# Performance work log

Hardware: AMD Instinct MI355X
Metric: run time of the kernel (lower is better)

Reference implementation:

```python
import jax, jax.numpy as jnp
import numpy as np

B, S, H = 1, 4096, 2048
HQ, HKV, D = 8, 4, 256
WIN = 1024          # sliding window
SOFTCAP = 50.0      # attn logit softcapping
EPS = 1e-6          # rms_norm_eps
ROPE_THETA = 10000.0


def setup_inputs() -> dict:
    key = jax.random.key(0)
    ks = jax.random.split(key, 6)
    hidden_states = jax.random.normal(ks[0], (B, S, H), dtype=jnp.float32)
    # RoPE cos/sin tables, shape [B, S, D]
    inv_freq = 1.0 / (ROPE_THETA ** (jnp.arange(0, D, 2, dtype=jnp.float32) / D))
    pos = jnp.arange(S, dtype=jnp.float32)
    freqs = pos[:, None] * inv_freq[None, :]          # [S, D/2]
    emb = jnp.concatenate([freqs, freqs], axis=-1)    # [S, D]
    cos = jnp.broadcast_to(jnp.cos(emb)[None], (B, S, D)).astype(jnp.float32)
    sin = jnp.broadcast_to(jnp.sin(emb)[None], (B, S, D)).astype(jnp.float32)
    qpos = jnp.arange(S)[:, None]
    kpos = jnp.arange(S)[None, :]
    diff = qpos - kpos
    allowed = (diff >= 0) & (diff < WIN)
    attention_mask = jnp.where(allowed, 0.0, -1e9).astype(jnp.float32)[None, None]
    attention_mask = jnp.broadcast_to(attention_mask, (B, 1, S, S))
    w_scale = 0.02
    Wq = jax.random.normal(ks[1], (HQ * D, H), dtype=jnp.float32) * w_scale
    Wk = jax.random.normal(ks[2], (HKV * D, H), dtype=jnp.float32) * w_scale
    Wv = jax.random.normal(ks[3], (HKV * D, H), dtype=jnp.float32) * w_scale
    Wo = jax.random.normal(ks[4], (H, HQ * D), dtype=jnp.float32) * w_scale
    q_norm_w = jnp.ones((D,), dtype=jnp.float32)
    k_norm_w = jnp.ones((D,), dtype=jnp.float32)
    return {"hidden_states": hidden_states, "cos": cos, "sin": sin,
            "attention_mask": attention_mask, "Wq": Wq, "Wk": Wk, "Wv": Wv,
            "Wo": Wo, "q_norm_w": q_norm_w, "k_norm_w": k_norm_w}


def _rms_norm(x, weight=None):
    # Gemma4 RMSNorm in fp32: x * rsqrt(mean(x^2) + eps) [* weight]
    ms = jnp.mean(x * x, axis=-1, keepdims=True) + EPS
    y = x * jax.lax.rsqrt(ms)
    return y * weight if weight is not None else y


def _rope(x, cos, sin):
    # x: [B,S,Hn,D]; cos/sin: [B,S,D] -> unsqueeze at dim 2
    x1, x2 = jnp.split(x, 2, axis=-1)
    rot = jnp.concatenate([-x2, x1], axis=-1)
    return x * cos[:, :, None, :] + rot * sin[:, :, None, :]


def reference(hidden_states, cos, sin, attention_mask, Wq, Wk, Wv, Wo, q_norm_w, k_norm_w):
    n_rep = HQ // HKV
    q = (hidden_states @ Wq.T).reshape(B, S, HQ, D)     # [B,S,HQ,D]
    q = _rms_norm(q, q_norm_w)
    q = _rope(q, cos, sin).transpose(0, 2, 1, 3)        # [B,HQ,S,D]
    k = (hidden_states @ Wk.T).reshape(B, S, HKV, D)
    k = _rms_norm(k, k_norm_w)
    k = _rope(k, cos, sin).transpose(0, 2, 1, 3)        # [B,HKV,S,D]
    v = (hidden_states @ Wv.T).reshape(B, S, HKV, D)
    v = _rms_norm(v).transpose(0, 2, 1, 3)              # [B,HKV,S,D]
    # repeat_kv (GQA)
    k = jnp.repeat(k, n_rep, axis=1)                    # [B,HQ,S,D]
    v = jnp.repeat(v, n_rep, axis=1)
    scores = jnp.einsum('bhqd,bhkd->bhqk', q, k)        # scaling = 1.0
    scores = jnp.tanh(scores / SOFTCAP) * SOFTCAP       # softcap
    scores = scores + attention_mask
    attn = jax.nn.softmax(scores.astype(jnp.float32), axis=-1).astype(q.dtype)
    out = jnp.einsum('bhqk,bhkd->bhqd', attn, v)        # [B,HQ,S,D]
    out = out.transpose(0, 2, 1, 3).reshape(B, S, HQ * D)
    return out @ Wo.T                                   # [B,S,H]
```

## Files before the change

### kernel.cpp

```cpp
#include <hip/hip_runtime.h>

#define S_LEN 4096
#define HID   2048
#define NHQ   8
#define NKV   4
#define DHEAD 256
#define WIN   1024

typedef __attribute__((ext_vector_type(4))) float     floatx4;
typedef __attribute__((ext_vector_type(8))) _Float16  halfx8;
typedef __attribute__((ext_vector_type(8))) __bf16    bf16x8;

__device__ __forceinline__ unsigned short f2h(float f){
  union { _Float16 h; unsigned short u; } cv; cv.h = (_Float16)f; return cv.u;
}
__device__ __forceinline__ float h2f(unsigned short u){
  union { unsigned short u; _Float16 h; } cv; cv.u = u; return (float)cv.h;
}
__device__ __forceinline__ unsigned short f2bf(float f){
  unsigned int u = __float_as_uint(f);
  u += 0x7FFFu + ((u >> 16) & 1u);
  return (unsigned short)(u >> 16);
}

__device__ __forceinline__ void gld_lds16(const void* g, void* l){
  __builtin_amdgcn_global_load_lds((const __attribute__((address_space(1))) void*)g,
                                   (__attribute__((address_space(3))) void*)l, 16, 0, 0);
}

__global__ __launch_bounds__(256) void cvt_all(const float* __restrict__ hs,
                                               const float* __restrict__ Wq,
                                               const float* __restrict__ Wk,
                                               const float* __restrict__ Wv,
                                               const float* __restrict__ Wo,
                                               unsigned short* __restrict__ h_h,
                                               unsigned short* __restrict__ w_qkv,
                                               unsigned short* __restrict__ wo){
  int bid = blockIdx.x;
  const float* src;
  unsigned short* dst;
  size_t i;
  if (bid < 8192){
    i = ((size_t)bid * 256 + threadIdx.x) * 4;
    src = hs + i; dst = h_h + i;
  } else if (bid < 16384){
    i = ((size_t)(bid - 8192) * 256 + threadIdx.x) * 4;
    int row = (int)(i >> 11), col = (int)(i & 2047);
    src = ((row < 2048) ? (Wq + ((size_t)row << 11))
         : (row < 3072) ? (Wk + ((size_t)(row - 2048) << 11))
                        : (Wv + ((size_t)(row - 3072) << 11))) + col;
    dst = w_qkv + i;
  } else {
    i = ((size_t)(bid - 16384) * 256 + threadIdx.x) * 4;
    src = Wo + i; dst = wo + i;
  }
  float4 v = *(const float4*)src;
  *(ushort4*)dst = make_ushort4(f2h(v.x), f2h(v.y), f2h(v.z), f2h(v.w));
}

template<int OUT_F32>
__global__ __launch_bounds__(256, 3) void gemm_cnt(const unsigned short* __restrict__ A,
                                                   const unsigned short* __restrict__ B,
                                                   void* __restrict__ Cv,
                                                   int ldC, int K, int nx){
  __shared__ __align__(16) unsigned short As[3][128 * 32];
  __shared__ __align__(16) unsigned short Bs[3][128 * 32];
  const int T = K >> 5;
  const int t0 = threadIdx.x, w = t0 >> 6, lane = t0 & 63;
  const int wm = w >> 1, wn = w & 1;
  const int quad = lane >> 4, l15 = lane & 15;
  const int qsw8 = ((quad ^ ((l15 >> 1) & 3)) << 3);

  const int nwg = (int)gridDim.x;
  const int wg = ((int)blockIdx.x & 7) * (nwg >> 3) + ((int)blockIdx.x >> 3);
  const int by = wg / nx, bx = wg - by * nx;
  const int bm0 = by * 128, bn0 = bx * 128;

  const int sr = t0 >> 2;
  const int swc8 = (((t0 & 3) ^ ((t0 >> 3) & 3)) << 3);
  const int ldst = sr * 32 + ((t0 & 3) << 3);
  const unsigned short* aG = A + (size_t)(bm0 + sr) * K + swc8;
  const unsigned short* bG = B + (size_t)(bn0 + sr) * K + swc8;

#define STAGE(U, SL) {                                                        \
    gld_lds16(aG + (size_t)(U) * 32,                  &As[SL][ldst]);         \
    gld_lds16(aG + (size_t)(U) * 32 + (size_t)64 * K, &As[SL][2048 + ldst]);  \
    gld_lds16(bG + (size_t)(U) * 32,                  &Bs[SL][ldst]);         \
    gld_lds16(bG + (size_t)(U) * 32 + (size_t)64 * K, &Bs[SL][2048 + ldst]); }

  STAGE(0, 0)
  STAGE(1, 1)
  asm volatile("s_waitcnt vmcnt(4)" ::: "memory");
  __builtin_amdgcn_s_barrier();

  const floatx4 zf = {0.f, 0.f, 0.f, 0.f};
  floatx4 acc[4][4];
#pragma unroll
  for (int mi = 0; mi < 4; ++mi)
#pragma unroll
    for (int ni = 0; ni < 4; ++ni) acc[mi][ni] = zf;

  int sl = 0;
  for (int t = 0; t < T; ++t){
    const unsigned short* Ap = &As[sl][0];
    const unsigned short* Bp = &Bs[sl][0];
    halfx8 af[4], bf[4];
#pragma unroll
    for (int mi = 0; mi < 4; ++mi) af[mi] = *(const halfx8*)&Ap[(wm*64 + mi*16 + l15)*32 + qsw8];
#pragma unroll
    for (int ni = 0; ni < 4; ++ni) bf[ni] = *(const halfx8*)&Bp[(wn*64 + ni*16 + l15)*32 + qsw8];
    if (t + 2 < T){
      const int sn = sl ? sl - 1 : 2;
      STAGE(t + 2, sn)
    }
    __builtin_amdgcn_s_setprio(1);
#pragma unroll
    for (int mi = 0; mi < 4; ++mi)
#pragma unroll
      for (int ni = 0; ni < 4; ++ni)
        acc[mi][ni] = __builtin_amdgcn_mfma_f32_16x16x32_f16(af[mi], bf[ni], acc[mi][ni], 0, 0, 0);
    __builtin_amdgcn_s_setprio(0);
    if (t < T - 2)       { asm volatile("s_waitcnt vmcnt(4)" ::: "memory"); }
    else if (t == T - 2) { asm volatile("s_waitcnt vmcnt(0)" ::: "memory"); }
    __builtin_amdgcn_s_barrier();
    sl = (sl == 2) ? 0 : sl + 1;
  }
#undef STAGE

#pragma unroll
  for (int mi = 0; mi < 4; ++mi)
#pragma unroll
    for (int ni = 0; ni < 4; ++ni)
#pragma unroll
      for (int r = 0; r < 4; ++r){
        int m = bm0 + wm*64 + mi*16 + quad*4 + r;
        int n = bn0 + wn*64 + ni*16 + l15;
        float v = acc[mi][ni][r];
        if (OUT_F32) ((float*)Cv)[(size_t)m * ldC + n] = v;
        else         ((unsigned short*)Cv)[(size_t)m * ldC + n] = f2h(v);
      }
}

__global__ __launch_bounds__(256) void qkv_post(const unsigned short* __restrict__ qkvh,
                                                const float* __restrict__ cosb,
                                                const float* __restrict__ sinb,
                                                const float* __restrict__ qnw,
                                                const float* __restrict__ knw,
                                                unsigned short* __restrict__ Qf,
                                                unsigned short* __restrict__ Kf,
                                                unsigned short* __restrict__ Vf){
  int gw   = blockIdx.x * 4 + (threadIdx.x >> 6);
  int lane = threadIdx.x & 63;
  int hh = gw & 15, s = gw >> 4;
  int colbase = (hh < 8) ? hh * 256 : (hh < 12 ? 2048 + (hh - 8) * 256 : 3072 + (hh - 12) * 256);

  ushort4 raw = *(const ushort4*)(qkvh + (size_t)s * 4096 + colbase + lane * 4);
  float x0 = h2f(raw.x), x1 = h2f(raw.y), x2 = h2f(raw.z), x3 = h2f(raw.w);
  float ss = x0*x0 + x1*x1 + x2*x2 + x3*x3;
#pragma unroll
  for (int off = 32; off; off >>= 1) ss += __shfl_xor(ss, off);
  float inv = rsqrtf(ss * (1.0f / 256.0f) + 1e-6f);

  if (hh < 12){
    const float* wp = (hh < 8) ? qnw : knw;
    float4 wv = *(const float4*)(wp + lane * 4);
    float y[4] = { x0*inv*wv.x, x1*inv*wv.y, x2*inv*wv.z, x3*inv*wv.w };
    float4 cv = *(const float4*)(cosb + (size_t)s * 256 + lane * 4);
    float4 sv = *(const float4*)(sinb + (size_t)s * 256 + lane * 4);
    float cj[4] = {cv.x, cv.y, cv.z, cv.w};
    float sj[4] = {sv.x, sv.y, sv.z, sv.w};
    unsigned short oh[4];
#pragma unroll
    for (int j = 0; j < 4; ++j){
      float oth = __shfl_xor(y[j], 32);
      float rot = (lane < 32) ? -oth : oth;
      oh[j] = f2h(y[j] * cj[j] + rot * sj[j]);
    }
    ushort4 r = make_ushort4(oh[0], oh[1], oh[2], oh[3]);
    if (hh < 8) *(ushort4*)(Qf + (size_t)(hh       * S_LEN + s) * DHEAD + lane * 4) = r;
    else        *(ushort4*)(Kf + (size_t)((hh - 8) * S_LEN + s) * DHEAD + lane * 4) = r;
  } else {
    ushort4 r = make_ushort4(f2bf(x0*inv), f2bf(x1*inv), f2bf(x2*inv), f2bf(x3*inv));
    *(ushort4*)(Vf + (size_t)((hh - 12) * S_LEN + s) * DHEAD + lane * 4) = r;
  }
}

__global__ __launch_bounds__(256) void transpose_v(const unsigned short* __restrict__ v,
                                                   unsigned short* __restrict__ vt){
  __shared__ unsigned short tile[64][68];
  int kv = blockIdx.z, d0 = blockIdx.x * 64, s0 = blockIdx.y * 64;
  int t = threadIdx.x;
  int r = t >> 4, c4 = (t & 15) * 4;
#pragma unroll
  for (int i = 0; i < 4; ++i){
    int row = r + i * 16;
    ushort4 xx = *(const ushort4*)(v + (size_t)(kv * S_LEN + s0 + row) * DHEAD + d0 + c4);
    tile[row][c4] = xx.x; tile[row][c4+1] = xx.y; tile[row][c4+2] = xx.z; tile[row][c4+3] = xx.w;
  }
  __syncthreads();
#pragma unroll
  for (int i = 0; i < 4; ++i){
    int dr = r + i * 16;
    ushort4 yy = make_ushort4(tile[c4][dr], tile[c4+1][dr], tile[c4+2][dr], tile[c4+3][dr]);
    *(ushort4*)(vt + (size_t)(kv * DHEAD + d0 + dr) * S_LEN + s0 + c4) = yy;
  }
}

__global__ __launch_bounds__(256, 2) void attn_win(const unsigned short* __restrict__ Qg,
                                                   const unsigned short* __restrict__ Kg,
                                                   const unsigned short* __restrict__ Vt,
                                                   unsigned short* __restrict__ Og){
  __shared__ __align__(16) unsigned short Ks[2][8 * 32 * 32];
  __shared__ __align__(16) unsigned short Vts[2][256 * 32];
  __shared__ __align__(16) unsigned short Pb[4][16 * 40];

  const int bid = blockIdx.x;
  const int h = bid & 7, kv = h >> 1;
  const int q0 = (bid >> 3) * 64;
  const int t = threadIdx.x, w = t >> 6, lane = t & 63;
  const int quad = lane >> 4, l15 = lane & 15;
  const int l2 = lane >> 2;
  const int gsw = (((lane & 3) ^ ((l2 >> 1) & 3)) << 3);
  const int qsw = ((quad ^ ((l15 >> 1) & 3)) << 3);
  const int qw0 = q0 + w * 16;

  halfx8 qf[8];
#pragma unroll
  for (int c = 0; c < 8; ++c)
    qf[c] = *(const halfx8*)(Qg + (size_t)(h * S_LEN + qw0 + l15) * DHEAD + c*32 + quad*8);

  const floatx4 zf = {0.f, 0.f, 0.f, 0.f};
  floatx4 oacc[16];
#pragma unroll
  for (int dt = 0; dt < 16; ++dt) oacc[dt] = zf;
  float l_part[4] = {0.f, 0.f, 0.f, 0.f};

  int kt_lo = q0 / 32 - 32; if (kt_lo < 0) kt_lo = 0;
  int kt_hi = q0 / 32 + 1;

  const size_t kbase = (size_t)kv * S_LEN * DHEAD;
  const size_t vbase = (size_t)kv * DHEAD * S_LEN;

#define STAGE(KT, B)                                                              \
  {                                                                               \
    const int key0_ = (KT) * 32;                                                  \
    _Pragma("unroll")                                                             \
    for (int j = 0; j < 4; ++j){                                                  \
      int ch = j * 4 + w;                                                         \
      int krow = (ch & 1) * 16 + l2;                                              \
      int cb = ch >> 1;                                                           \
      gld_lds16(Kg + kbase + (size_t)(key0_ + krow) * DHEAD + cb * 32 + gsw,      \
                &Ks[B][ch * 512]);                                                \
      int drow = ch * 16 + l2;                                                    \
      gld_lds16(Vt + vbase + (size_t)drow * S_LEN + key0_ + gsw,                  \
                &Vts[B][ch * 512]);                                               \
    }                                                                             \
  }

  STAGE(kt_lo, 0);

  for (int kt = kt_lo; kt <= kt_hi; ++kt){
    const int cur = (kt - kt_lo) & 1;
    if (kt < kt_hi){
      STAGE(kt + 1, cur ^ 1);
      asm volatile("s_waitcnt vmcnt(8)" ::: "memory");
    } else {
      asm volatile("s_waitcnt vmcnt(0)" ::: "memory");
    }
    __builtin_amdgcn_s_barrier();

    const int key0 = kt * 32;
    if (key0 <= qw0 + 15 && key0 + 31 >= qw0 - (WIN - 1)){
      floatx4 sc[2];
      sc[0] = zf; sc[1] = zf;
      __builtin_amdgcn_s_setprio(1);
#pragma unroll
      for (int c = 0; c < 8; ++c){
#pragma unroll
        for (int nt = 0; nt < 2; ++nt){
          halfx8 kf = *(const halfx8*)&Ks[cur][c * 1024 + (nt*16 + l15) * 32 + qsw];
          sc[nt] = __builtin_amdgcn_mfma_f32_16x16x32_f16(qf[c], kf, sc[nt], 0, 0, 0);
        }
      }
      __builtin_amdgcn_s_setprio(0);
      const bool tfull = (key0 + 31 <= qw0) && (qw0 + 15 - key0 < WIN);
#pragma unroll
      for (int nt = 0; nt < 2; ++nt)
#pragma unroll
        for (int r = 0; r < 4; ++r){
          float v = sc[nt][r];
          float e  = __builtin_amdgcn_exp2f(v * 0.0577078016f);
          float tt = __builtin_amdgcn_rcpf(e + 1.0f);
          float p  = __builtin_amdgcn_exp2f(fmaf(tt, -144.26950408f, 28.8539008f));
          if (!tfull){
            int qi = qw0 + quad*4 + r;
            int ki = key0 + nt*16 + l15;
            p = ((ki <= qi) && (qi - ki < WIN)) ? p : 0.0f;
          }
          l_part[r] += p;
          Pb[w][(quad*4 + r) * 40 + nt*16 + l15] = f2bf(p);
        }
      bf16x8 pf = *(const bf16x8*)&Pb[w][l15 * 40 + quad * 8];
      __builtin_amdgcn_s_setprio(1);
#pragma unroll
      for (int dt = 0; dt < 16; ++dt){
        bf16x8 vf = *(const bf16x8*)&Vts[cur][(dt*16 + l15) * 32 + qsw];
        oacc[dt] = __builtin_amdgcn_mfma_f32_16x16x32_bf16(pf, vf, oacc[dt], 0, 0, 0);
      }
      __builtin_amdgcn_s_setprio(0);
    }
    __builtin_amdgcn_s_barrier();
  }
#undef STAGE

#pragma unroll
  for (int r = 0; r < 4; ++r){
    float l = l_part[r];
    l += __shfl_xor(l, 1);
    l += __shfl_xor(l, 2);
    l += __shfl_xor(l, 4);
    l += __shfl_xor(l, 8);
    float rl = 1.0f / l;
    int srow = qw0 + quad*4 + r;
#pragma unroll
    for (int dt = 0; dt < 16; ++dt)
      Og[(size_t)srow * (NHQ * DHEAD) + h * DHEAD + dt*16 + l15] = f2h(oacc[dt][r] * rl);
  }
}

extern "C" void kernel_launch(void* const* d_in, const int* in_sizes, int n_in,
                              void* d_out, int out_size, void* d_ws, size_t ws_size,
                              hipStream_t stream){
  const float* hs   = (const float*)d_in[0];
  const float* cosb = (const float*)d_in[1];
  const float* sinb = (const float*)d_in[2];
  const float* Wq   = (const float*)d_in[4];
  const float* Wk   = (const float*)d_in[5];
  const float* Wv   = (const float*)d_in[6];
  const float* Wo   = (const float*)d_in[7];
  const float* qnw  = (const float*)d_in[8];
  const float* knw  = (const float*)d_in[9];
  float* out = (float*)d_out;

  const size_t MB = 1024ull * 1024ull;
  char* ws = (char*)d_ws;
  unsigned short* h_h   = (unsigned short*)(ws);
  unsigned short* w_qkv = (unsigned short*)(ws + 16 * MB);
  unsigned short* wo    = (unsigned short*)(ws + 32 * MB);
  unsigned short* qkvh  = (unsigned short*)(ws + 40 * MB);
  unsigned short* Qf    = (unsigned short*)(ws);
  unsigned short* Kf    = (unsigned short*)(ws + 16 * MB);
  unsigned short* Vf    = (unsigned short*)(ws + 24 * MB);
  unsigned short* vt    = (unsigned short*)(ws + 40 * MB);
  unsigned short* ob    = (unsigned short*)(ws + 48 * MB);

  cvt_all<<<20480, 256, 0, stream>>>(hs, Wq, Wk, Wv, Wo, h_h, w_qkv, wo);

  gemm_cnt<0><<<1024, 256, 0, stream>>>(h_h, w_qkv, qkvh, 4096, 2048, 32);

  qkv_post<<<16384, 256, 0, stream>>>(qkvh, cosb, sinb, qnw, knw, Qf, Kf, Vf);
  transpose_v<<<dim3(4, 64, 4), 256, 0, stream>>>(Vf, vt);

  attn_win<<<512, 256, 0, stream>>>(Qf, Kf, vt, ob);

  gemm_cnt<1><<<512, 256, 0, stream>>>(ob, wo, out, 2048, 2048, 16);
}
```

Before: 404.9 us.

## Restructure fp16 GEMM to double-buffered BK=64 tiles with split LDS waits

Reworks the projection GEMM mainloop from a 3-stage BK=32 pipeline to a 2-stage BK=64 double buffer with a new XOR swizzle. Each iteration now does two MFMA batches, and the second batch waits on its LDS reads only after the first batch has been issued. The blockIdx remapping for L2 locality is dropped and occupancy is lowered to 2 waves per SIMD. This cuts barrier count per unit of K, at the cost of pipeline depth, occupancy and cache-friendly tile ordering.

```diff
diff --git a/kernel.cpp b/kernel.cpp
--- a/kernel.cpp
+++ b/kernel.cpp
@@ -59,39 +59,36 @@
 }
 
 template<int OUT_F32>
-__global__ __launch_bounds__(256, 3) void gemm_cnt(const unsigned short* __restrict__ A,
+__global__ __launch_bounds__(256, 2) void gemm_cnt(const unsigned short* __restrict__ A,
                                                    const unsigned short* __restrict__ B,
                                                    void* __restrict__ Cv,
                                                    int ldC, int K, int nx){
-  __shared__ __align__(16) unsigned short As[3][128 * 32];
-  __shared__ __align__(16) unsigned short Bs[3][128 * 32];
-  const int T = K >> 5;
+  __shared__ __align__(16) unsigned short As[2][128 * 64];
+  __shared__ __align__(16) unsigned short Bs[2][128 * 64];
+  const int T = K >> 6;
   const int t0 = threadIdx.x, w = t0 >> 6, lane = t0 & 63;
   const int wm = w >> 1, wn = w & 1;
   const int quad = lane >> 4, l15 = lane & 15;
-  const int qsw8 = ((quad ^ ((l15 >> 1) & 3)) << 3);
-
-  const int nwg = (int)gridDim.x;
-  const int wg = ((int)blockIdx.x & 7) * (nwg >> 3) + ((int)blockIdx.x >> 3);
+
+  const int wg = (int)blockIdx.x;
   const int by = wg / nx, bx = wg - by * nx;
   const int bm0 = by * 128, bn0 = bx * 128;
 
-  const int sr = t0 >> 2;
-  const int swc8 = (((t0 & 3) ^ ((t0 >> 3) & 3)) << 3);
-  const int ldst = sr * 32 + ((t0 & 3) << 3);
-  const unsigned short* aG = A + (size_t)(bm0 + sr) * K + swc8;
-  const unsigned short* bG = B + (size_t)(bn0 + sr) * K + swc8;
-
-#define STAGE(U, SL) {                                                        \
-    gld_lds16(aG + (size_t)(U) * 32,                  &As[SL][ldst]);         \
-    gld_lds16(aG + (size_t)(U) * 32 + (size_t)64 * K, &As[SL][2048 + ldst]);  \
-    gld_lds16(bG + (size_t)(U) * 32,                  &Bs[SL][ldst]);         \
-    gld_lds16(bG + (size_t)(U) * 32 + (size_t)64 * K, &Bs[SL][2048 + ldst]); }
-
-  STAGE(0, 0)
-  STAGE(1, 1)
-  asm volatile("s_waitcnt vmcnt(4)" ::: "memory");
-  __builtin_amdgcn_s_barrier();
+  const int grow = lane >> 3;
+  const int sg8  = (((lane & 7) ^ grow) << 3);
+
+#define STG(U, SL) {                                                          \
+    _Pragma("unroll")                                                         \
+    for (int j = 0; j < 4; ++j){                                              \
+      const int ch = w + 4 * j;                                               \
+      const int gr = ch * 8 + grow;                                           \
+      gld_lds16(A + (size_t)(bm0 + gr) * K + (size_t)(U) * 64 + sg8,          \
+                &As[SL][ch * 512]);                                           \
+      gld_lds16(B + (size_t)(bn0 + gr) * K + (size_t)(U) * 64 + sg8,          \
+                &Bs[SL][ch * 512]);                                           \
+    } }
+
+  STG(0, 0)
 
   const floatx4 zf = {0.f, 0.f, 0.f, 0.f};
   floatx4 acc[4][4];
@@ -100,32 +97,54 @@
 #pragma unroll
     for (int ni = 0; ni < 4; ++ni) acc[mi][ni] = zf;
 
-  int sl = 0;
   for (int t = 0; t < T; ++t){
-    const unsigned short* Ap = &As[sl][0];
-    const unsigned short* Bp = &Bs[sl][0];
-    halfx8 af[4], bf[4];
-#pragma unroll
-    for (int mi = 0; mi < 4; ++mi) af[mi] = *(const halfx8*)&Ap[(wm*64 + mi*16 + l15)*32 + qsw8];
-#pragma unroll
-    for (int ni = 0; ni < 4; ++ni) bf[ni] = *(const halfx8*)&Bp[(wn*64 + ni*16 + l15)*32 + qsw8];
-    if (t + 2 < T){
-      const int sn = sl ? sl - 1 : 2;
-      STAGE(t + 2, sn)
-    }
+    const int cur = t & 1;
+    if (t + 1 < T){
+      STG(t + 1, cur ^ 1)
+      asm volatile("s_waitcnt vmcnt(8)" ::: "memory");
+    } else {
+      asm volatile("s_waitcnt vmcnt(0)" ::: "memory");
+    }
+    __builtin_amdgcn_s_barrier();
+    __builtin_amdgcn_sched_barrier(0);
+
+    halfx8 af[4][2], bf[4][2];
+#pragma unroll
+    for (int mi = 0; mi < 4; ++mi){
+      const int r = wm * 64 + mi * 16 + l15;
+      const int s0 = (quad ^ (r & 7)) << 3;
+      af[mi][0] = *(const halfx8*)&As[cur][r * 64 + s0];
+      af[mi][1] = *(const halfx8*)&As[cur][r * 64 + (s0 ^ 32)];
+    }
+#pragma unroll
+    for (int ni = 0; ni < 4; ++ni){
+      const int r = wn * 64 + ni * 16 + l15;
+      const int s0 = (quad ^ (r & 7)) << 3;
+      bf[ni][0] = *(const halfx8*)&Bs[cur][r * 64 + s0];
+      bf[ni][1] = *(const halfx8*)&Bs[cur][r * 64 + (s0 ^ 32)];
+    }
+    asm volatile("s_waitcnt lgkmcnt(8)" ::: "memory");
+    __builtin_amdgcn_sched_barrier(0);
     __builtin_amdgcn_s_setprio(1);
 #pragma unroll
     for (int mi = 0; mi < 4; ++mi)
 #pragma unroll
       for (int ni = 0; ni < 4; ++ni)
-        acc[mi][ni] = __builtin_amdgcn_mfma_f32_16x16x32_f16(af[mi], bf[ni], acc[mi][ni], 0, 0, 0);
+        acc[mi][ni] = __builtin_amdgcn_mfma_f32_16x16x32_f16(af[mi][0], bf[ni][0], acc[mi][ni], 0, 0, 0);
     __builtin_amdgcn_s_setprio(0);
-    if (t < T - 2)       { asm volatile("s_waitcnt vmcnt(4)" ::: "memory"); }
-    else if (t == T - 2) { asm volatile("s_waitcnt vmcnt(0)" ::: "memory"); }
+    asm volatile("s_waitcnt lgkmcnt(0)" ::: "memory");
+    __builtin_amdgcn_sched_barrier(0);
+    __builtin_amdgcn_s_setprio(1);
+#pragma unroll
+    for (int mi = 0; mi < 4; ++mi)
+#pragma unroll
+      for (int ni = 0; ni < 4; ++ni)
+        acc[mi][ni] = __builtin_amdgcn_mfma_f32_16x16x32_f16(af[mi][1], bf[ni][1], acc[mi][ni], 0, 0, 0);
+    __builtin_amdgcn_s_setprio(0);
     __builtin_amdgcn_s_barrier();
-    sl = (sl == 2) ? 0 : sl + 1;
-  }
-#undef STAGE
+    __builtin_amdgcn_sched_barrier(0);
+  }
+#undef STG
 
 #pragma unroll
   for (int mi = 0; mi < 4; ++mi)
```

Result: faster. 381.6 us (-5.8%).
